# Kernel tuning notes

Hardware: AMD Instinct MI355X
Metric: run time of the kernel (lower is better)

Reference implementation:

```python
import jax, jax.numpy as jnp
import numpy as np

F = 32          # fmap_size = (256 // 16) * 2
WIN = F // 8 - 1  # window = 3
HID = 160
HID4 = 640
N = 4096
Q = 16


def setup_inputs() -> dict:
    key = jax.random.key(0)
    ks = jax.random.split(key, 24)

    def lin(k, i, o):
        return jax.random.normal(k, (i, o), jnp.float32) * (1.0 / np.sqrt(i))

    return {
        "feature_pos": jax.random.normal(ks[0], (N, Q, HID), jnp.float32),
        "query_embedding": jax.random.normal(ks[1], (N, Q, HID), jnp.float32),
        "attn_matrix": jax.random.normal(ks[2], (N, Q, F * F), jnp.float32),
        "ws1": lin(ks[3], HID, HID4), "bs1": jnp.zeros((HID4,), jnp.float32),
        "ws2": lin(ks[4], HID4, HID4), "bs2": jnp.zeros((HID4,), jnp.float32),
        "ws3": lin(ks[5], HID4, HID4), "bs3": jnp.zeros((HID4,), jnp.float32),
        "ws4": lin(ks[6], HID4, 1), "bs4": jnp.zeros((1,), jnp.float32),
        "wp1": lin(ks[7], HID, HID4), "bp1": jnp.zeros((HID4,), jnp.float32),
        "wp2": lin(ks[8], HID4, HID4), "bp2": jnp.zeros((HID4,), jnp.float32),
        "wp3": lin(ks[9], HID4, HID4), "bp3": jnp.zeros((HID4,), jnp.float32),
        "wp4": lin(ks[10], HID4, 4), "bp4": jnp.zeros((4,), jnp.float32),
    }


def _mlp(x, w1, b1, w2, b2, w3, b3, w4, b4):
    h = jax.nn.relu(x @ w1 + b1)
    h = jax.nn.relu(h @ w2 + b2)
    h = jax.nn.relu(h @ w3 + b3)
    return h @ w4 + b4


def _gauss_blur3(x):
    # torchvision GaussianBlur(3, sigma=1.0): separable 3-tap, reflect padding
    e = np.exp(-0.5)
    k = jnp.asarray([e, 1.0, e], jnp.float32) / np.float32(1.0 + 2.0 * e)
    xp = jnp.pad(x, ((0, 0), (1, 1), (0, 0)), mode="reflect")
    x = k[0] * xp[:, :-2] + k[1] * xp[:, 1:-1] + k[2] * xp[:, 2:]
    xp = jnp.pad(x, ((0, 0), (0, 0), (1, 1)), mode="reflect")
    return k[0] * xp[:, :, :-2] + k[1] * xp[:, :, 1:-1] + k[2] * xp[:, :, 2:]


def _process_attnmap(am):
    # am: [N, F, F]
    n = am.shape[0]
    ab = _gauss_blur3(am)
    ab = (ab - ab.mean(axis=(1, 2), keepdims=True)) / jnp.std(ab, axis=(1, 2), keepdims=True, ddof=1)
    idx = jnp.argmax(ab.reshape(n, -1), axis=1)
    px = (idx % F).astype(jnp.int32)
    py = (idx // F).astype(jnp.int32)
    # vectorized windowed mean of clamped sigmoid (masked instead of per-sample slicing)
    s = jnp.clip(jax.nn.sigmoid(am), 1e-4, 1.0 - 1e-4)
    pos = jnp.arange(F)
    colmask = ((pos[None, :] >= jnp.maximum(0, px - WIN)[:, None]) &
               (pos[None, :] < jnp.minimum(F, px + WIN)[:, None])).astype(s.dtype)  # [N,F]
    rowmask = ((pos[None, :] >= jnp.maximum(0, py - WIN)[:, None]) &
               (pos[None, :] < jnp.minimum(F, py + WIN)[:, None])).astype(s.dtype)
    colsum = s.sum(axis=1)  # [N,F] sum over rows -> per-column totals
    rowsum = s.sum(axis=2)  # [N,F] sum over cols -> per-row totals
    tempx = (colsum * colmask).sum(axis=1) / (F * colmask.sum(axis=1))
    tempy = (rowsum * rowmask).sum(axis=1) / (F * rowmask.sum(axis=1))
    prepos = jnp.stack([px, py], axis=1).astype(jnp.float32)          # [N,2]
    presize = jnp.stack([tempx, tempy], axis=1) * np.float32(F)        # [N,2]
    return prepos, presize


def reference(feature_pos, query_embedding, attn_matrix,
              ws1, bs1, ws2, bs2, ws3, bs3, ws4, bs4,
              wp1, bp1, wp2, bp2, wp3, bp3, wp4, bp4):
    n = query_embedding.shape[0]
    qe = query_embedding.mean(axis=1)   # [N, HID]
    fp = feature_pos.mean(axis=1)       # [N, HID]
    am = attn_matrix.mean(axis=1).reshape(n, F, F)
    score = _mlp(qe, ws1, bs1, ws2, bs2, ws3, bs3, ws4, bs4).reshape(n)
    bbox_info = _mlp(fp, wp1, bp1, wp2, bp2, wp3, bp3, wp4, bp4)  # [N,4]
    sizeoffset = jnp.clip(bbox_info[:, :2], -2.0, 2.0)
    posoffset = jnp.clip(bbox_info[:, 2:], -2.0, 2.0)
    prepos, presize = _process_attnmap(am)
    xy = (prepos + posoffset) / np.float32(F)
    wh = (presize + sizeoffset) / np.float32(F)
    xy = xy - 0.5 * wh  # predict_center
    bbox = jnp.concatenate([xy, wh], axis=1)
    return bbox, score
```

## Files before the change

kernel.cpp:

```cpp
#include <hip/hip_runtime.h>
#include <hip/hip_bf16.h>
#include <stdint.h>

#define HID 160
#define HID4 640
#define FDIM 32
#define NPIX 1024

#define GK0 0.27406862f
#define GK1 0.45186276f

typedef __attribute__((ext_vector_type(8))) short short8;
typedef __attribute__((ext_vector_type(4))) float f32x4;

__device__ __forceinline__ ushort f2b(float f) {
  union { float f; uint32_t u; } v; v.f = f;
  uint32_t u = v.u;
  u += 0x7fffu + ((u >> 16) & 1u);
  return (ushort)(u >> 16);
}
__device__ __forceinline__ float b2f(ushort s) {
  union { uint32_t u; float f; } v; v.u = ((uint32_t)s) << 16;
  return v.f;
}

__device__ __forceinline__ void gload16(const ushort* g, ushort* l) {
  __builtin_amdgcn_global_load_lds(
      (const __attribute__((address_space(1))) void*)g,
      (__attribute__((address_space(3))) void*)l, 16, 0, 0);
}

union SMem {
  struct {
    ushort la[128 * 32];
    ushort lb[128 * 32];
  } g;
  struct {
    float am[FDIM][FDIM + 1];
    float tmp[FDIM][FDIM + 1];
    float bl[FDIM][FDIM + 1];
    float rowsum[FDIM], colsum[FDIM];
    float redv[4];
    int redi[4];
  } a;
};

__device__ void attn_block(SMem& sm, const float* __restrict__ attn,
                           float* __restrict__ pp, int n) {
  const int tid = threadIdx.x;
  const float* base = attn + (size_t)n * (16 * NPIX);
  float4 a = make_float4(0.f, 0.f, 0.f, 0.f);
#pragma unroll
  for (int q = 0; q < 16; ++q) {
    float4 v = *(const float4*)(base + q * NPIX + tid * 4);
    a.x += v.x; a.y += v.y; a.z += v.z; a.w += v.w;
  }
  {
    const int f0 = tid * 4;
    const int r = f0 >> 5, c = f0 & 31;
    sm.a.am[r][c + 0] = a.x * 0.0625f;
    sm.a.am[r][c + 1] = a.y * 0.0625f;
    sm.a.am[r][c + 2] = a.z * 0.0625f;
    sm.a.am[r][c + 3] = a.w * 0.0625f;
  }
  __syncthreads();
  for (int f = tid; f < NPIX; f += 256) {
    int r = f >> 5, c = f & 31;
    int rm = (r == 0) ? 1 : r - 1;
    int rp = (r == 31) ? 30 : r + 1;
    sm.a.tmp[r][c] = GK0 * sm.a.am[rm][c] + GK1 * sm.a.am[r][c] + GK0 * sm.a.am[rp][c];
  }
  __syncthreads();
  for (int f = tid; f < NPIX; f += 256) {
    int r = f >> 5, c = f & 31;
    int cm = (c == 0) ? 1 : c - 1;
    int cp = (c == 31) ? 30 : c + 1;
    sm.a.bl[r][c] = GK0 * sm.a.tmp[r][cm] + GK1 * sm.a.tmp[r][c] + GK0 * sm.a.tmp[r][cp];
  }
  __syncthreads();
  float bv = -1e30f; int bi = 0;
  for (int f = tid; f < NPIX; f += 256) {
    float v = sm.a.bl[f >> 5][f & 31];
    if (v > bv || (v == bv && f < bi)) { bv = v; bi = f; }
  }
  for (int off = 32; off > 0; off >>= 1) {
    float ov = __shfl_down(bv, off);
    int oi = __shfl_down(bi, off);
    if (ov > bv || (ov == bv && oi < bi)) { bv = ov; bi = oi; }
  }
  if ((tid & 63) == 0) { sm.a.redv[tid >> 6] = bv; sm.a.redi[tid >> 6] = bi; }
  for (int f = tid; f < NPIX; f += 256) {
    int r = f >> 5, c = f & 31;
    float s = 1.f / (1.f + expf(-sm.a.am[r][c]));
    sm.a.tmp[r][c] = fminf(fmaxf(s, 1e-4f), 0.9999f);
  }
  __syncthreads();
  if (tid < 32) {
    float s = 0.f;
    for (int c = 0; c < 32; ++c) s += sm.a.tmp[tid][c];
    sm.a.rowsum[tid] = s;
  } else if (tid < 64) {
    int c = tid - 32;
    float s = 0.f;
    for (int r = 0; r < 32; ++r) s += sm.a.tmp[r][c];
    sm.a.colsum[c] = s;
  }
  __syncthreads();
  if (tid == 0) {
    float bestv = sm.a.redv[0]; int besti = sm.a.redi[0];
    for (int w = 1; w < 4; ++w)
      if (sm.a.redv[w] > bestv || (sm.a.redv[w] == bestv && sm.a.redi[w] < besti)) {
        bestv = sm.a.redv[w]; besti = sm.a.redi[w];
      }
    int px = besti & 31, py = besti >> 5;
    int c0 = max(0, px - 3), c1 = min(32, px + 3);
    float sx = 0.f;
    for (int c = c0; c < c1; ++c) sx += sm.a.colsum[c];
    float psx = (sx / (32.f * (float)(c1 - c0))) * 32.f;
    int r0 = max(0, py - 3), r1 = min(32, py + 3);
    float sy = 0.f;
    for (int r = r0; r < r1; ++r) sy += sm.a.rowsum[r];
    float psy = (sy / (32.f * (float)(r1 - r0))) * 32.f;
    pp[n * 4 + 0] = (float)px;
    pp[n * 4 + 1] = (float)py;
    pp[n * 4 + 2] = psx;
    pp[n * 4 + 3] = psy;
  }
}

template <int K>
__global__ __launch_bounds__(256) void gemm_attn(
    const ushort* __restrict__ A0, const ushort* __restrict__ A1,
    const ushort* __restrict__ W0, const ushort* __restrict__ W1,
    const float* __restrict__ B0, const float* __restrict__ B1,
    ushort* __restrict__ O0, ushort* __restrict__ O1,
    const float* __restrict__ attn, float* __restrict__ pp,
    int attn_base, int n_gemm) {
  __shared__ SMem sm;
  const int tid = threadIdx.x;

  if ((int)blockIdx.x >= n_gemm) {
    attn_block(sm, attn, pp, attn_base + (int)blockIdx.x - n_gemm);
    return;
  }

  const int bid = blockIdx.x;
  const int half = n_gemm >> 1;
  const int chain = bid >= half;
  const int r = chain ? bid - half : bid;
  const int bn = (r % 5) * 128;
  const int bm = (r / 5) * 128;
  const ushort* A = chain ? A1 : A0;
  const ushort* W = chain ? W1 : W0;
  const float* bias = chain ? B1 : B0;
  ushort* O = chain ? O1 : O0;

  const int lane = tid & 63;
  const int wid = tid >> 6;
  const int wr = (wid >> 1) * 64;
  const int wc = (wid & 1) * 64;
  const int l15 = lane & 15;
  const int kq = (lane >> 4) * 8;

  const int rstage = tid >> 2;
  const int cstage = (tid & 3) * 8;
  ushort* la = sm.g.la;
  ushort* lb = sm.g.lb;
  const int ldsbase = wid * 512;

  f32x4 acc[4][4] = {};
  for (int k0 = 0; k0 < K; k0 += 32) {
#pragma unroll
    for (int j = 0; j < 2; ++j) {
      gload16(A + (size_t)(bm + j * 64 + rstage) * K + k0 + cstage,
              la + j * 2048 + ldsbase);
      gload16(W + (size_t)(bn + j * 64 + rstage) * K + k0 + cstage,
              lb + j * 2048 + ldsbase);
    }
    __syncthreads();
    short8 af[4], bf[4];
#pragma unroll
    for (int i = 0; i < 4; ++i) {
      af[i] = *(const short8*)(la + (wr + i * 16 + l15) * 32 + kq);
      bf[i] = *(const short8*)(lb + (wc + i * 16 + l15) * 32 + kq);
    }
#pragma unroll
    for (int mi = 0; mi < 4; ++mi)
#pragma unroll
      for (int nj = 0; nj < 4; ++nj)
        acc[mi][nj] = __builtin_amdgcn_mfma_f32_16x16x32_bf16(af[mi], bf[nj], acc[mi][nj], 0, 0, 0);
    __syncthreads();
  }

#pragma unroll
  for (int nj = 0; nj < 4; ++nj) {
    const int col = bn + wc + nj * 16 + l15;
    const float bcol = bias[col];
#pragma unroll
    for (int mi = 0; mi < 4; ++mi) {
      const int rbase = bm + wr + mi * 16 + (lane >> 4) * 4;
#pragma unroll
      for (int b = 0; b < 4; ++b) {
        float v = acc[mi][nj][b] + bcol;
        O[(size_t)(rbase + b) * HID4 + col] = f2b(fmaxf(v, 0.f));
      }
    }
  }
}

__global__ __launch_bounds__(256) void prep_kernel(
    const float* __restrict__ qemb, const float* __restrict__ fpos,
    ushort* __restrict__ qe_b, ushort* __restrict__ fp_b,
    const float* __restrict__ ws1, ushort* __restrict__ wts1,
    const float* __restrict__ wp1, ushort* __restrict__ wtp1,
    const float* __restrict__ ws2, ushort* __restrict__ wts2,
    const float* __restrict__ wp2, ushort* __restrict__ wtp2,
    const float* __restrict__ ws3, ushort* __restrict__ wts3,
    const float* __restrict__ wp3, ushort* __restrict__ wtp3,
    int n_mean_blocks, int total) {
  const int tid = threadIdx.x;
  const int bid = blockIdx.x;

  if (bid < n_mean_blocks) {
    int idx = bid * 256 + tid;
    const int pairs = total >> 1;
    const float* src; ushort* dst; int i;
    if (idx < pairs) { src = qemb; dst = qe_b; i = idx; }
    else             { src = fpos; dst = fp_b; i = idx - pairs; }
    int nn = i / (HID / 2);
    int h = (i - nn * (HID / 2)) * 2;
    const float* p = src + (size_t)nn * (16 * HID) + h;
    float sx = 0.f, sy = 0.f;
#pragma unroll
    for (int q = 0; q < 16; ++q) {
      float2 v = *(const float2*)(p + q * HID);
      sx += v.x; sy += v.y;
    }
    ushort2 o;
    o.x = f2b(sx * 0.0625f);
    o.y = f2b(sy * 0.0625f);
    *(ushort2*)(dst + (size_t)nn * HID + h) = o;
    return;
  }

  int r = bid - n_mean_blocks;
  const float* in; ushort* out; int K;
  if (r < 100)       { in = ws1; out = wts1; K = HID; }
  else if (r < 200)  { in = wp1; out = wtp1; K = HID; r -= 100; }
  else if (r < 600)  { in = ws2; out = wts2; K = HID4; r -= 200; }
  else if (r < 1000) { in = wp2; out = wtp2; K = HID4; r -= 600; }
  else if (r < 1400) { in = ws3; out = wts3; K = HID4; r -= 1000; }
  else               { in = wp3; out = wtp3; K = HID4; r -= 1400; }
  const int bx = (r % 20) * 32;
  const int by = (r / 20) * 32;
  const int lx = tid & 31;
  const int ly = tid >> 5;
  __shared__ float t[32][33];
#pragma unroll
  for (int i = 0; i < 4; ++i)
    t[ly + i * 8][lx] = in[(size_t)(by + ly + i * 8) * HID4 + bx + lx];
  __syncthreads();
#pragma unroll
  for (int i = 0; i < 4; ++i)
    out[(size_t)(bx + ly + i * 8) * K + by + lx] = f2b(t[lx][ly + i * 8]);
}

__global__ __launch_bounds__(256) void final_kernel(
    const ushort* __restrict__ hs, const ushort* __restrict__ hp,
    const float* __restrict__ ws4, const float* __restrict__ bs4,
    const float* __restrict__ wp4, const float* __restrict__ bp4,
    const float* __restrict__ pp, float* __restrict__ out, int N) {
  const int wid = threadIdx.x >> 6;
  const int lane = threadIdx.x & 63;
  const int n = blockIdx.x * 4 + wid;
  if (n >= N) return;
  const ushort* hsr = hs + (size_t)n * HID4;
  const ushort* hpr = hp + (size_t)n * HID4;
  float sc = 0.f, b0 = 0.f, b1 = 0.f, b2 = 0.f, b3 = 0.f;
  for (int j = lane; j < HID4; j += 64) {
    float h1 = b2f(hsr[j]);
    sc += h1 * ws4[j];
    float h2 = b2f(hpr[j]);
    b0 += h2 * wp4[j * 4 + 0];
    b1 += h2 * wp4[j * 4 + 1];
    b2 += h2 * wp4[j * 4 + 2];
    b3 += h2 * wp4[j * 4 + 3];
  }
  for (int off = 32; off > 0; off >>= 1) {
    sc += __shfl_down(sc, off);
    b0 += __shfl_down(b0, off);
    b1 += __shfl_down(b1, off);
    b2 += __shfl_down(b2, off);
    b3 += __shfl_down(b3, off);
  }
  if (lane == 0) {
    sc += bs4[0];
    b0 += bp4[0]; b1 += bp4[1]; b2 += bp4[2]; b3 += bp4[3];
    float so0 = fminf(fmaxf(b0, -2.f), 2.f);
    float so1 = fminf(fmaxf(b1, -2.f), 2.f);
    float po0 = fminf(fmaxf(b2, -2.f), 2.f);
    float po1 = fminf(fmaxf(b3, -2.f), 2.f);
    float px = pp[n * 4 + 0], py = pp[n * 4 + 1];
    float psx = pp[n * 4 + 2], psy = pp[n * 4 + 3];
    float wh0 = (psx + so0) * (1.f / 32.f);
    float wh1 = (psy + so1) * (1.f / 32.f);
    float xy0 = (px + po0) * (1.f / 32.f) - 0.5f * wh0;
    float xy1 = (py + po1) * (1.f / 32.f) - 0.5f * wh1;
    out[n * 4 + 0] = xy0;
    out[n * 4 + 1] = xy1;
    out[n * 4 + 2] = wh0;
    out[n * 4 + 3] = wh1;
    out[(size_t)4 * N + n] = sc;
  }
}

extern "C" void kernel_launch(void* const* d_in, const int* in_sizes, int n_in,
                              void* d_out, int out_size, void* d_ws, size_t ws_size,
                              hipStream_t stream) {
  const float* fpos = (const float*)d_in[0];
  const float* qemb = (const float*)d_in[1];
  const float* attn = (const float*)d_in[2];
  const float* ws1 = (const float*)d_in[3];
  const float* bs1 = (const float*)d_in[4];
  const float* ws2 = (const float*)d_in[5];
  const float* bs2 = (const float*)d_in[6];
  const float* ws3 = (const float*)d_in[7];
  const float* bs3 = (const float*)d_in[8];
  const float* ws4 = (const float*)d_in[9];
  const float* bs4 = (const float*)d_in[10];
  const float* wp1 = (const float*)d_in[11];
  const float* bp1 = (const float*)d_in[12];
  const float* wp2 = (const float*)d_in[13];
  const float* bp2 = (const float*)d_in[14];
  const float* wp3 = (const float*)d_in[15];
  const float* bp3 = (const float*)d_in[16];
  const float* wp4 = (const float*)d_in[17];
  const float* bp4 = (const float*)d_in[18];
  float* out = (float*)d_out;

  const int N = in_sizes[0] / (16 * HID);

  char* ws = (char*)d_ws;
  const size_t SZ_QE = (size_t)N * HID * 2;
  const size_t SZ_W1 = (size_t)HID4 * HID * 2;
  const size_t SZ_W2 = (size_t)HID4 * HID4 * 2;
  const size_t SZ_H  = (size_t)N * HID4 * 2;
  size_t off = 0;
  ushort* qe_b = (ushort*)(ws + off); off += SZ_QE;
  ushort* fp_b = (ushort*)(ws + off); off += SZ_QE;
  ushort* wts1 = (ushort*)(ws + off); off += SZ_W1;
  ushort* wtp1 = (ushort*)(ws + off); off += SZ_W1;
  ushort* wts2 = (ushort*)(ws + off); off += SZ_W2;
  ushort* wtp2 = (ushort*)(ws + off); off += SZ_W2;
  ushort* wts3 = (ushort*)(ws + off); off += SZ_W2;
  ushort* wtp3 = (ushort*)(ws + off); off += SZ_W2;
  ushort* hsA  = (ushort*)(ws + off); off += SZ_H;
  ushort* hsB  = (ushort*)(ws + off); off += SZ_H;
  ushort* hpA  = (ushort*)(ws + off); off += SZ_H;
  ushort* hpB  = (ushort*)(ws + off); off += SZ_H;
  float*  pp   = (float*)(ws + off);  off += (size_t)N * 4 * 4;

  const int total = N * HID;
  const int n_mean_blocks = (2 * (total >> 1) + 255) / 256;
  prep_kernel<<<n_mean_blocks + 1800, 256, 0, stream>>>(
      qemb, fpos, qe_b, fp_b, ws1, wts1, wp1, wtp1, ws2, wts2, wp2, wtp2,
      ws3, wts3, wp3, wtp3, n_mean_blocks, total);

  const int n_gemm = 2 * 5 * (N / 128);
  const int a2 = (N * 29) / 100;
  const int a3 = a2;
  const int a1 = N - a2 - a3;

  gemm_attn<HID><<<n_gemm + a1, 256, 0, stream>>>(
      qe_b, fp_b, wts1, wtp1, bs1, bp1, hsA, hpA, attn, pp, 0, n_gemm);
  gemm_attn<HID4><<<n_gemm + a2, 256, 0, stream>>>(
      hsA, hpA, wts2, wtp2, bs2, bp2, hsB, hpB, attn, pp, a1, n_gemm);
  gemm_attn<HID4><<<n_gemm + a3, 256, 0, stream>>>(
      hsB, hpB, wts3, wtp3, bs3, bp3, hsA, hpA, attn, pp, a1 + a2, n_gemm);

  final_kernel<<<(N + 3) / 4, 256, 0, stream>>>(hsA, hpA, ws4, bs4, wp4, bp4, pp, out, N);
}
```

Measured before the change: 119.4 us.

## Double-buffer GEMM LDS loads, swizzle layout, halve N tile, rebalance attn blocks

The GEMM main loop now double-buffers its LDS tiles, issuing the next K-slice's global-to-LDS loads before computing on the current one and using explicit waitcnt plus barriers. It also XOR-swizzles the LDS layout to cut bank conflicts and shrinks the N tile from 128 to 64, which doubles the GEMM block count. The attention-map blocks are redistributed across four launches, with a share moved into the prep kernel. The cost is more LDS per block and more A-tile reloads, in exchange for better latency hiding and load balance.

```diff
diff --git a/kernel.cpp b/kernel.cpp
--- a/kernel.cpp
+++ b/kernel.cpp
@@ -30,22 +30,29 @@
       (__attribute__((address_space(3))) void*)l, 16, 0, 0);
 }
 
-union SMem {
+struct AttnSM {
+  float am[FDIM][FDIM + 1];
+  float tmp[FDIM][FDIM + 1];
+  float bl[FDIM][FDIM + 1];
+  float rowsum[FDIM], colsum[FDIM];
+  float redv[4];
+  int redi[4];
+};
+
+union GemmSM {
   struct {
-    ushort la[128 * 32];
-    ushort lb[128 * 32];
+    ushort la[2][4096];
+    ushort lb[2][2048];
   } g;
-  struct {
-    float am[FDIM][FDIM + 1];
-    float tmp[FDIM][FDIM + 1];
-    float bl[FDIM][FDIM + 1];
-    float rowsum[FDIM], colsum[FDIM];
-    float redv[4];
-    int redi[4];
-  } a;
+  AttnSM a;
 };
 
-__device__ void attn_block(SMem& sm, const float* __restrict__ attn,
+union PrepSM {
+  float t[32][33];
+  AttnSM a;
+};
+
+__device__ void attn_block(AttnSM& sm, const float* __restrict__ attn,
                            float* __restrict__ pp, int n) {
   const int tid = threadIdx.x;
   const float* base = attn + (size_t)n * (16 * NPIX);
@@ -58,29 +65,29 @@
   {
     const int f0 = tid * 4;
     const int r = f0 >> 5, c = f0 & 31;
-    sm.a.am[r][c + 0] = a.x * 0.0625f;
-    sm.a.am[r][c + 1] = a.y * 0.0625f;
-    sm.a.am[r][c + 2] = a.z * 0.0625f;
-    sm.a.am[r][c + 3] = a.w * 0.0625f;
+    sm.am[r][c + 0] = a.x * 0.0625f;
+    sm.am[r][c + 1] = a.y * 0.0625f;
+    sm.am[r][c + 2] = a.z * 0.0625f;
+    sm.am[r][c + 3] = a.w * 0.0625f;
   }
   __syncthreads();
   for (int f = tid; f < NPIX; f += 256) {
     int r = f >> 5, c = f & 31;
     int rm = (r == 0) ? 1 : r - 1;
     int rp = (r == 31) ? 30 : r + 1;
-    sm.a.tmp[r][c] = GK0 * sm.a.am[rm][c] + GK1 * sm.a.am[r][c] + GK0 * sm.a.am[rp][c];
+    sm.tmp[r][c] = GK0 * sm.am[rm][c] + GK1 * sm.am[r][c] + GK0 * sm.am[rp][c];
   }
   __syncthreads();
   for (int f = tid; f < NPIX; f += 256) {
     int r = f >> 5, c = f & 31;
     int cm = (c == 0) ? 1 : c - 1;
     int cp = (c == 31) ? 30 : c + 1;
-    sm.a.bl[r][c] = GK0 * sm.a.tmp[r][cm] + GK1 * sm.a.tmp[r][c] + GK0 * sm.a.tmp[r][cp];
+    sm.bl[r][c] = GK0 * sm.tmp[r][cm] + GK1 * sm.tmp[r][c] + GK0 * sm.tmp[r][cp];
   }
   __syncthreads();
   float bv = -1e30f; int bi = 0;
   for (int f = tid; f < NPIX; f += 256) {
-    float v = sm.a.bl[f >> 5][f & 31];
+    float v = sm.bl[f >> 5][f & 31];
     if (v > bv || (v == bv && f < bi)) { bv = v; bi = f; }
   }
   for (int off = 32; off > 0; off >>= 1) {
@@ -88,38 +95,38 @@
     int oi = __shfl_down(bi, off);
     if (ov > bv || (ov == bv && oi < bi)) { bv = ov; bi = oi; }
   }
-  if ((tid & 63) == 0) { sm.a.redv[tid >> 6] = bv; sm.a.redi[tid >> 6] = bi; }
+  if ((tid & 63) == 0) { sm.redv[tid >> 6] = bv; sm.redi[tid >> 6] = bi; }
   for (int f = tid; f < NPIX; f += 256) {
     int r = f >> 5, c = f & 31;
-    float s = 1.f / (1.f + expf(-sm.a.am[r][c]));
-    sm.a.tmp[r][c] = fminf(fmaxf(s, 1e-4f), 0.9999f);
+    float s = 1.f / (1.f + expf(-sm.am[r][c]));
+    sm.tmp[r][c] = fminf(fmaxf(s, 1e-4f), 0.9999f);
   }
   __syncthreads();
   if (tid < 32) {
     float s = 0.f;
-    for (int c = 0; c < 32; ++c) s += sm.a.tmp[tid][c];
-    sm.a.rowsum[tid] = s;
+    for (int c = 0; c < 32; ++c) s += sm.tmp[tid][c];
+    sm.rowsum[tid] = s;
   } else if (tid < 64) {
     int c = tid - 32;
     float s = 0.f;
-    for (int r = 0; r < 32; ++r) s += sm.a.tmp[r][c];
-    sm.a.colsum[c] = s;
+    for (int r = 0; r < 32; ++r) s += sm.tmp[r][c];
+    sm.colsum[c] = s;
   }
   __syncthreads();
   if (tid == 0) {
-    float bestv = sm.a.redv[0]; int besti = sm.a.redi[0];
+    float bestv = sm.redv[0]; int besti = sm.redi[0];
     for (int w = 1; w < 4; ++w)
-      if (sm.a.redv[w] > bestv || (sm.a.redv[w] == bestv && sm.a.redi[w] < besti)) {
-        bestv = sm.a.redv[w]; besti = sm.a.redi[w];
+      if (sm.redv[w] > bestv || (sm.redv[w] == bestv && sm.redi[w] < besti)) {
+        bestv = sm.redv[w]; besti = sm.redi[w];
       }
     int px = besti & 31, py = besti >> 5;
     int c0 = max(0, px - 3), c1 = min(32, px + 3);
     float sx = 0.f;
-    for (int c = c0; c < c1; ++c) sx += sm.a.colsum[c];
+    for (int c = c0; c < c1; ++c) sx += sm.colsum[c];
     float psx = (sx / (32.f * (float)(c1 - c0))) * 32.f;
     int r0 = max(0, py - 3), r1 = min(32, py + 3);
     float sy = 0.f;
-    for (int r = r0; r < r1; ++r) sy += sm.a.rowsum[r];
+    for (int r = r0; r < r1; ++r) sy += sm.rowsum[r];
     float psy = (sy / (32.f * (float)(r1 - r0))) * 32.f;
     pp[n * 4 + 0] = (float)px;
     pp[n * 4 + 1] = (float)py;
@@ -136,11 +143,11 @@
     ushort* __restrict__ O0, ushort* __restrict__ O1,
     const float* __restrict__ attn, float* __restrict__ pp,
     int attn_base, int n_gemm) {
-  __shared__ SMem sm;
+  __shared__ GemmSM sm;
   const int tid = threadIdx.x;
 
   if ((int)blockIdx.x >= n_gemm) {
-    attn_block(sm, attn, pp, attn_base + (int)blockIdx.x - n_gemm);
+    attn_block(sm.a, attn, pp, attn_base + (int)blockIdx.x - n_gemm);
     return;
   }
 
@@ -148,8 +155,8 @@
   const int half = n_gemm >> 1;
   const int chain = bid >= half;
   const int r = chain ? bid - half : bid;
-  const int bn = (r % 5) * 128;
-  const int bm = (r / 5) * 128;
+  const int bn = (r % 10) * 64;
+  const int bm = (r / 10) * 128;
   const ushort* A = chain ? A1 : A0;
   const ushort* W = chain ? W1 : W0;
   const float* bias = chain ? B1 : B0;
@@ -158,42 +165,67 @@
   const int lane = tid & 63;
   const int wid = tid >> 6;
   const int wr = (wid >> 1) * 64;
-  const int wc = (wid & 1) * 64;
+  const int wc = (wid & 1) * 32;
   const int l15 = lane & 15;
   const int kq = (lane >> 4) * 8;
 
   const int rstage = tid >> 2;
   const int cstage = (tid & 3) * 8;
-  ushort* la = sm.g.la;
-  ushort* lb = sm.g.lb;
-  const int ldsbase = wid * 512;
-
-  f32x4 acc[4][4] = {};
-  for (int k0 = 0; k0 < K; k0 += 32) {
-#pragma unroll
-    for (int j = 0; j < 2; ++j) {
-      gload16(A + (size_t)(bm + j * 64 + rstage) * K + k0 + cstage,
-              la + j * 2048 + ldsbase);
-      gload16(W + (size_t)(bn + j * 64 + rstage) * K + k0 + cstage,
-              lb + j * 2048 + ldsbase);
+  const int cs_sw = cstage ^ ((rstage & 6) << 2);
+
+  ushort* la = &sm.g.la[0][0];
+  ushort* lb = &sm.g.lb[0][0];
+  const int ldsw = wid * 512;
+
+  const size_t arow0 = (size_t)(bm + rstage) * K + cs_sw;
+  const size_t arow1 = (size_t)(bm + 64 + rstage) * K + cs_sw;
+  const size_t brow  = (size_t)(bn + rstage) * K + cs_sw;
+
+  gload16(A + arow0, la + ldsw);
+  gload16(A + arow1, la + 2048 + ldsw);
+  gload16(W + brow,  lb + ldsw);
+
+  constexpr int NT = K / 32;
+  f32x4 acc[4][2] = {};
+  for (int t = 0; t < NT; ++t) {
+    const int cur = t & 1;
+    if (t + 1 < NT) {
+      const int k1 = (t + 1) * 32;
+      const int nxt = cur ^ 1;
+      gload16(A + arow0 + k1, la + nxt * 4096 + ldsw);
+      gload16(A + arow1 + k1, la + nxt * 4096 + 2048 + ldsw);
+      gload16(W + brow + k1,  lb + nxt * 2048 + ldsw);
+      asm volatile("s_waitcnt vmcnt(3)" ::: "memory");
+    } else {
+      asm volatile("s_waitcnt vmcnt(0)" ::: "memory");
     }
-    __syncthreads();
-    short8 af[4], bf[4];
-#pragma unroll
-    for (int i = 0; i < 4; ++i) {
-      af[i] = *(const short8*)(la + (wr + i * 16 + l15) * 32 + kq);
-      bf[i] = *(const short8*)(lb + (wc + i * 16 + l15) * 32 + kq);
+    __builtin_amdgcn_s_barrier();
+
+    const ushort* lac = la + cur * 4096;
+    const ushort* lbc = lb + cur * 2048;
+    short8 af[4], bf[2];
+#pragma unroll
+    for (int mi = 0; mi < 4; ++mi) {
+      const int rr = wr + mi * 16 + l15;
+      af[mi] = *(const short8*)(lac + rr * 32 + (kq ^ ((rr & 6) << 2)));
     }
 #pragma unroll
+    for (int nj = 0; nj < 2; ++nj) {
+      const int rr = wc + nj * 16 + l15;
+      bf[nj] = *(const short8*)(lbc + rr * 32 + (kq ^ ((rr & 6) << 2)));
+    }
+#pragma unroll
     for (int mi = 0; mi < 4; ++mi)
 #pragma unroll
-      for (int nj = 0; nj < 4; ++nj)
+      for (int nj = 0; nj < 2; ++nj)
         acc[mi][nj] = __builtin_amdgcn_mfma_f32_16x16x32_bf16(af[mi], bf[nj], acc[mi][nj], 0, 0, 0);
-    __syncthreads();
-  }
-
-#pragma unroll
-  for (int nj = 0; nj < 4; ++nj) {
+
+    asm volatile("s_waitcnt lgkmcnt(0)" ::: "memory");
+    __builtin_amdgcn_s_barrier();
+  }
+
+#pragma unroll
+  for (int nj = 0; nj < 2; ++nj) {
     const int col = bn + wc + nj * 16 + l15;
     const float bcol = bias[col];
 #pragma unroll
@@ -217,7 +249,9 @@
     const float* __restrict__ wp2, ushort* __restrict__ wtp2,
     const float* __restrict__ ws3, ushort* __restrict__ wts3,
     const float* __restrict__ wp3, ushort* __restrict__ wtp3,
-    int n_mean_blocks, int total) {
+    const float* __restrict__ attn, float* __restrict__ pp,
+    int n_mean_blocks, int n_trans_blocks, int total) {
+  __shared__ PrepSM sm;
   const int tid = threadIdx.x;
   const int bid = blockIdx.x;
 
@@ -243,26 +277,30 @@
     return;
   }
 
-  int r = bid - n_mean_blocks;
-  const float* in; ushort* out; int K;
-  if (r < 100)       { in = ws1; out = wts1; K = HID; }
-  else if (r < 200)  { in = wp1; out = wtp1; K = HID; r -= 100; }
-  else if (r < 600)  { in = ws2; out = wts2; K = HID4; r -= 200; }
-  else if (r < 1000) { in = wp2; out = wtp2; K = HID4; r -= 600; }
-  else if (r < 1400) { in = ws3; out = wts3; K = HID4; r -= 1000; }
-  else               { in = wp3; out = wtp3; K = HID4; r -= 1400; }
-  const int bx = (r % 20) * 32;
-  const int by = (r / 20) * 32;
-  const int lx = tid & 31;
-  const int ly = tid >> 5;
-  __shared__ float t[32][33];
-#pragma unroll
-  for (int i = 0; i < 4; ++i)
-    t[ly + i * 8][lx] = in[(size_t)(by + ly + i * 8) * HID4 + bx + lx];
-  __syncthreads();
-#pragma unroll
-  for (int i = 0; i < 4; ++i)
-    out[(size_t)(bx + ly + i * 8) * K + by + lx] = f2b(t[lx][ly + i * 8]);
+  if (bid < n_mean_blocks + n_trans_blocks) {
+    int r = bid - n_mean_blocks;
+    const float* in; ushort* out; int K;
+    if (r < 100)       { in = ws1; out = wts1; K = HID; }
+    else if (r < 200)  { in = wp1; out = wtp1; K = HID; r -= 100; }
+    else if (r < 600)  { in = ws2; out = wts2; K = HID4; r -= 200; }
+    else if (r < 1000) { in = wp2; out = wtp2; K = HID4; r -= 600; }
+    else if (r < 1400) { in = ws3; out = wts3; K = HID4; r -= 1000; }
+    else               { in = wp3; out = wtp3; K = HID4; r -= 1400; }
+    const int bx = (r % 20) * 32;
+    const int by = (r / 20) * 32;
+    const int lx = tid & 31;
+    const int ly = tid >> 5;
+#pragma unroll
+    for (int i = 0; i < 4; ++i)
+      sm.t[ly + i * 8][lx] = in[(size_t)(by + ly + i * 8) * HID4 + bx + lx];
+    __syncthreads();
+#pragma unroll
+    for (int i = 0; i < 4; ++i)
+      out[(size_t)(bx + ly + i * 8) * K + by + lx] = f2b(sm.t[lx][ly + i * 8]);
+    return;
+  }
+
+  attn_block(sm.a, attn, pp, bid - n_mean_blocks - n_trans_blocks);
 }
 
 __global__ __launch_bounds__(256) void final_kernel(
@@ -360,23 +398,26 @@
   ushort* hpB  = (ushort*)(ws + off); off += SZ_H;
   float*  pp   = (float*)(ws + off);  off += (size_t)N * 4 * 4;
 
+  const int a0 = (N * 25) / 64;
+  const int a1 = (N * 11) / 64;
+  const int a2 = (N * 14) / 64;
+  const int a3 = N - a0 - a1 - a2;
+
   const int total = N * HID;
-  const int n_mean_blocks = (2 * (total >> 1) + 255) / 256;
-  prep_kernel<<<n_mean_blocks + 1800, 256, 0, stream>>>(
+  const int n_mean = (total + 255) / 256;
+  const int n_trans = 1800;
+  prep_kernel<<<n_mean + n_trans + a0, 256, 0, stream>>>(
       qemb, fpos, qe_b, fp_b, ws1, wts1, wp1, wtp1, ws2, wts2, wp2, wtp2,
-      ws3, wts3, wp3, wtp3, n_mean_blocks, total);
-
-  const int n_gemm = 2 * 5 * (N / 128);
-  const int a2 = (N * 29) / 100;
-  const int a3 = a2;
-  const int a1 = N - a2 - a3;
+      ws3, wts3, wp3, wtp3, attn, pp, n_mean, n_trans, total);
+
+  const int n_gemm = 2 * (N / 128) * (HID4 / 64);
 
   gemm_attn<HID><<<n_gemm + a1, 256, 0, stream>>>(
-      qe_b, fp_b, wts1, wtp1, bs1, bp1, hsA, hpA, attn, pp, 0, n_gemm);
+      qe_b, fp_b, wts1, wtp1, bs1, bp1, hsA, hpA, attn, pp, a0, n_gemm);
   gemm_attn<HID4><<<n_gemm + a2, 256, 0, stream>>>(
-      hsA, hpA, wts2, wtp2, bs2, bp2, hsB, hpB, attn, pp, a1, n_gemm);
+      hsA, hpA, wts2, wtp2, bs2, bp2, hsB, hpB, attn, pp, a0 + a1, n_gemm);
   gemm_attn<HID4><<<n_gemm + a3, 256, 0, stream>>>(
-      hsB, hpB, wts3, wtp3, bs3, bp3, hsA, hpA, attn, pp, a1 + a2, n_gemm);
+      hsB, hpB, wts3, wtp3, bs3, bp3, hsA, hpA, attn, pp, a0 + a1 + a2, n_gemm);
 
   final_kernel<<<(N + 3) / 4, 256, 0, stream>>>(hsA, hpA, ws4, bs4, wp4, bp4, pp, out, N);
 }
```

After: 131.8 us. 10.4% more time.

## Process four attention maps per block with register prefetch of the next map

Applied to the files above, without the earlier changes.

Each attention block now handles four consecutive samples instead of one. While the current map is being processed in shared memory, the block loads the next sample's 16 query rows into registers, so global loads overlap with the blur, argmax and sigmoid work. This cuts the number of attention blocks by four and amortises per-block launch overhead, but it raises register pressure (16 float4 buffers) and lengthens each block's serial work, which could hurt overlap with the co-scheduled GEMM blocks. The remaining edits are cosmetic reorganisation of shared memory and launch arithmetic.

```diff
diff --git a/kernel.cpp b/kernel.cpp
--- a/kernel.cpp
+++ b/kernel.cpp
@@ -30,101 +30,130 @@
       (__attribute__((address_space(3))) void*)l, 16, 0, 0);
 }
 
-union SMem {
+struct AttnSM {
+  float am[FDIM][FDIM + 1];
+  float tmp[FDIM][FDIM + 1];
+  float bl[FDIM][FDIM + 1];
+  float rowsum[FDIM], colsum[FDIM];
+  float redv[4];
+  int redi[4];
+};
+
+union GemmSM {
   struct {
     ushort la[128 * 32];
     ushort lb[128 * 32];
   } g;
-  struct {
-    float am[FDIM][FDIM + 1];
-    float tmp[FDIM][FDIM + 1];
-    float bl[FDIM][FDIM + 1];
-    float rowsum[FDIM], colsum[FDIM];
-    float redv[4];
-    int redi[4];
-  } a;
+  AttnSM a;
 };
 
-__device__ void attn_block(SMem& sm, const float* __restrict__ attn,
-                           float* __restrict__ pp, int n) {
+__device__ void attn_multi(AttnSM& sm, const float* __restrict__ attn,
+                           float* __restrict__ pp, int n0, int cnt) {
   const int tid = threadIdx.x;
-  const float* base = attn + (size_t)n * (16 * NPIX);
-  float4 a = make_float4(0.f, 0.f, 0.f, 0.f);
-#pragma unroll
-  for (int q = 0; q < 16; ++q) {
-    float4 v = *(const float4*)(base + q * NPIX + tid * 4);
-    a.x += v.x; a.y += v.y; a.z += v.z; a.w += v.w;
-  }
+  float4 buf[16];
   {
-    const int f0 = tid * 4;
-    const int r = f0 >> 5, c = f0 & 31;
-    sm.a.am[r][c + 0] = a.x * 0.0625f;
-    sm.a.am[r][c + 1] = a.y * 0.0625f;
-    sm.a.am[r][c + 2] = a.z * 0.0625f;
-    sm.a.am[r][c + 3] = a.w * 0.0625f;
-  }
-  __syncthreads();
-  for (int f = tid; f < NPIX; f += 256) {
-    int r = f >> 5, c = f & 31;
-    int rm = (r == 0) ? 1 : r - 1;
-    int rp = (r == 31) ? 30 : r + 1;
-    sm.a.tmp[r][c] = GK0 * sm.a.am[rm][c] + GK1 * sm.a.am[r][c] + GK0 * sm.a.am[rp][c];
-  }
-  __syncthreads();
-  for (int f = tid; f < NPIX; f += 256) {
-    int r = f >> 5, c = f & 31;
-    int cm = (c == 0) ? 1 : c - 1;
-    int cp = (c == 31) ? 30 : c + 1;
-    sm.a.bl[r][c] = GK0 * sm.a.tmp[r][cm] + GK1 * sm.a.tmp[r][c] + GK0 * sm.a.tmp[r][cp];
-  }
-  __syncthreads();
-  float bv = -1e30f; int bi = 0;
-  for (int f = tid; f < NPIX; f += 256) {
-    float v = sm.a.bl[f >> 5][f & 31];
-    if (v > bv || (v == bv && f < bi)) { bv = v; bi = f; }
-  }
-  for (int off = 32; off > 0; off >>= 1) {
-    float ov = __shfl_down(bv, off);
-    int oi = __shfl_down(bi, off);
-    if (ov > bv || (ov == bv && oi < bi)) { bv = ov; bi = oi; }
-  }
-  if ((tid & 63) == 0) { sm.a.redv[tid >> 6] = bv; sm.a.redi[tid >> 6] = bi; }
-  for (int f = tid; f < NPIX; f += 256) {
-    int r = f >> 5, c = f & 31;
-    float s = 1.f / (1.f + expf(-sm.a.am[r][c]));
-    sm.a.tmp[r][c] = fminf(fmaxf(s, 1e-4f), 0.9999f);
-  }
-  __syncthreads();
-  if (tid < 32) {
-    float s = 0.f;
-    for (int c = 0; c < 32; ++c) s += sm.a.tmp[tid][c];
-    sm.a.rowsum[tid] = s;
-  } else if (tid < 64) {
-    int c = tid - 32;
-    float s = 0.f;
-    for (int r = 0; r < 32; ++r) s += sm.a.tmp[r][c];
-    sm.a.colsum[c] = s;
-  }
-  __syncthreads();
-  if (tid == 0) {
-    float bestv = sm.a.redv[0]; int besti = sm.a.redi[0];
-    for (int w = 1; w < 4; ++w)
-      if (sm.a.redv[w] > bestv || (sm.a.redv[w] == bestv && sm.a.redi[w] < besti)) {
-        bestv = sm.a.redv[w]; besti = sm.a.redi[w];
-      }
-    int px = besti & 31, py = besti >> 5;
-    int c0 = max(0, px - 3), c1 = min(32, px + 3);
-    float sx = 0.f;
-    for (int c = c0; c < c1; ++c) sx += sm.a.colsum[c];
-    float psx = (sx / (32.f * (float)(c1 - c0))) * 32.f;
-    int r0 = max(0, py - 3), r1 = min(32, py + 3);
-    float sy = 0.f;
-    for (int r = r0; r < r1; ++r) sy += sm.a.rowsum[r];
-    float psy = (sy / (32.f * (float)(r1 - r0))) * 32.f;
-    pp[n * 4 + 0] = (float)px;
-    pp[n * 4 + 1] = (float)py;
-    pp[n * 4 + 2] = psx;
-    pp[n * 4 + 3] = psy;
+    const float* b0 = attn + (size_t)n0 * (16 * NPIX) + tid * 4;
+#pragma unroll
+    for (int q = 0; q < 16; ++q) buf[q] = *(const float4*)(b0 + q * NPIX);
+  }
+
+  for (int s = 0; s < cnt; ++s) {
+    float4 a;
+#pragma unroll
+    for (int q = 8; q < 16; ++q) {
+      buf[q - 8].x += buf[q].x; buf[q - 8].y += buf[q].y;
+      buf[q - 8].z += buf[q].z; buf[q - 8].w += buf[q].w;
+    }
+#pragma unroll
+    for (int q = 4; q < 8; ++q) {
+      buf[q - 4].x += buf[q].x; buf[q - 4].y += buf[q].y;
+      buf[q - 4].z += buf[q].z; buf[q - 4].w += buf[q].w;
+    }
+    a.x = (buf[0].x + buf[2].x) + (buf[1].x + buf[3].x);
+    a.y = (buf[0].y + buf[2].y) + (buf[1].y + buf[3].y);
+    a.z = (buf[0].z + buf[2].z) + (buf[1].z + buf[3].z);
+    a.w = (buf[0].w + buf[2].w) + (buf[1].w + buf[3].w);
+
+    {
+      const int f0 = tid * 4;
+      const int r = f0 >> 5, c = f0 & 31;
+      sm.am[r][c + 0] = a.x * 0.0625f;
+      sm.am[r][c + 1] = a.y * 0.0625f;
+      sm.am[r][c + 2] = a.z * 0.0625f;
+      sm.am[r][c + 3] = a.w * 0.0625f;
+    }
+    __syncthreads();
+
+    if (s + 1 < cnt) {
+      const float* nb = attn + (size_t)(n0 + s + 1) * (16 * NPIX) + tid * 4;
+#pragma unroll
+      for (int q = 0; q < 16; ++q) buf[q] = *(const float4*)(nb + q * NPIX);
+    }
+
+    const int n = n0 + s;
+    for (int f = tid; f < NPIX; f += 256) {
+      int r = f >> 5, c = f & 31;
+      int rm = (r == 0) ? 1 : r - 1;
+      int rp = (r == 31) ? 30 : r + 1;
+      sm.tmp[r][c] = GK0 * sm.am[rm][c] + GK1 * sm.am[r][c] + GK0 * sm.am[rp][c];
+    }
+    __syncthreads();
+    for (int f = tid; f < NPIX; f += 256) {
+      int r = f >> 5, c = f & 31;
+      int cm = (c == 0) ? 1 : c - 1;
+      int cp = (c == 31) ? 30 : c + 1;
+      sm.bl[r][c] = GK0 * sm.tmp[r][cm] + GK1 * sm.tmp[r][c] + GK0 * sm.tmp[r][cp];
+    }
+    __syncthreads();
+    float bv = -1e30f; int bi = 0;
+    for (int f = tid; f < NPIX; f += 256) {
+      float v = sm.bl[f >> 5][f & 31];
+      if (v > bv || (v == bv && f < bi)) { bv = v; bi = f; }
+    }
+    for (int off = 32; off > 0; off >>= 1) {
+      float ov = __shfl_down(bv, off);
+      int oi = __shfl_down(bi, off);
+      if (ov > bv || (ov == bv && oi < bi)) { bv = ov; bi = oi; }
+    }
+    if ((tid & 63) == 0) { sm.redv[tid >> 6] = bv; sm.redi[tid >> 6] = bi; }
+    for (int f = tid; f < NPIX; f += 256) {
+      int r = f >> 5, c = f & 31;
+      float sg = 1.f / (1.f + expf(-sm.am[r][c]));
+      sm.tmp[r][c] = fminf(fmaxf(sg, 1e-4f), 0.9999f);
+    }
+    __syncthreads();
+    if (tid < 32) {
+      float ss = 0.f;
+      for (int c = 0; c < 32; ++c) ss += sm.tmp[tid][c];
+      sm.rowsum[tid] = ss;
+    } else if (tid < 64) {
+      int c = tid - 32;
+      float ss = 0.f;
+      for (int r = 0; r < 32; ++r) ss += sm.tmp[r][c];
+      sm.colsum[c] = ss;
+    }
+    __syncthreads();
+    if (tid == 0) {
+      float bestv = sm.redv[0]; int besti = sm.redi[0];
+      for (int w = 1; w < 4; ++w)
+        if (sm.redv[w] > bestv || (sm.redv[w] == bestv && sm.redi[w] < besti)) {
+          bestv = sm.redv[w]; besti = sm.redi[w];
+        }
+      int px = besti & 31, py = besti >> 5;
+      int c0 = max(0, px - 3), c1 = min(32, px + 3);
+      float sx = 0.f;
+      for (int c = c0; c < c1; ++c) sx += sm.colsum[c];
+      float psx = (sx / (32.f * (float)(c1 - c0))) * 32.f;
+      int r0 = max(0, py - 3), r1 = min(32, py + 3);
+      float sy = 0.f;
+      for (int r = r0; r < r1; ++r) sy += sm.rowsum[r];
+      float psy = (sy / (32.f * (float)(r1 - r0))) * 32.f;
+      pp[n * 4 + 0] = (float)px;
+      pp[n * 4 + 1] = (float)py;
+      pp[n * 4 + 2] = psx;
+      pp[n * 4 + 3] = psy;
+    }
+    __syncthreads();
   }
 }
 
@@ -135,12 +164,14 @@
     const float* __restrict__ B0, const float* __restrict__ B1,
     ushort* __restrict__ O0, ushort* __restrict__ O1,
     const float* __restrict__ attn, float* __restrict__ pp,
-    int attn_base, int n_gemm) {
-  __shared__ SMem sm;
+    int attn_base, int attn_cnt, int n_gemm) {
+  __shared__ GemmSM sm;
   const int tid = threadIdx.x;
 
   if ((int)blockIdx.x >= n_gemm) {
-    attn_block(sm, attn, pp, attn_base + (int)blockIdx.x - n_gemm);
+    const int n0 = attn_base + ((int)blockIdx.x - n_gemm) * 4;
+    const int cnt = min(4, attn_base + attn_cnt - n0);
+    attn_multi(sm.a, attn, pp, n0, cnt);
     return;
   }
 
@@ -218,6 +249,7 @@
     const float* __restrict__ ws3, ushort* __restrict__ wts3,
     const float* __restrict__ wp3, ushort* __restrict__ wtp3,
     int n_mean_blocks, int total) {
+  __shared__ float t[32][33];
   const int tid = threadIdx.x;
   const int bid = blockIdx.x;
 
@@ -255,7 +287,6 @@
   const int by = (r / 20) * 32;
   const int lx = tid & 31;
   const int ly = tid >> 5;
-  __shared__ float t[32][33];
 #pragma unroll
   for (int i = 0; i < 4; ++i)
     t[ly + i * 8][lx] = in[(size_t)(by + ly + i * 8) * HID4 + bx + lx];
@@ -361,22 +392,27 @@
   float*  pp   = (float*)(ws + off);  off += (size_t)N * 4 * 4;
 
   const int total = N * HID;
-  const int n_mean_blocks = (2 * (total >> 1) + 255) / 256;
-  prep_kernel<<<n_mean_blocks + 1800, 256, 0, stream>>>(
+  const int n_mean = (total + 255) / 256;
+  const int n_trans = 1800;
+  prep_kernel<<<n_mean + n_trans, 256, 0, stream>>>(
       qemb, fpos, qe_b, fp_b, ws1, wts1, wp1, wtp1, ws2, wts2, wp2, wtp2,
-      ws3, wts3, wp3, wtp3, n_mean_blocks, total);
-
-  const int n_gemm = 2 * 5 * (N / 128);
+      ws3, wts3, wp3, wtp3, n_mean, total);
+
+  const int n_gemm = 2 * (N / 128) * (HID4 / 128);
+
   const int a2 = (N * 29) / 100;
   const int a3 = a2;
   const int a1 = N - a2 - a3;
-
-  gemm_attn<HID><<<n_gemm + a1, 256, 0, stream>>>(
-      qe_b, fp_b, wts1, wtp1, bs1, bp1, hsA, hpA, attn, pp, 0, n_gemm);
-  gemm_attn<HID4><<<n_gemm + a2, 256, 0, stream>>>(
-      hsA, hpA, wts2, wtp2, bs2, bp2, hsB, hpB, attn, pp, a1, n_gemm);
-  gemm_attn<HID4><<<n_gemm + a3, 256, 0, stream>>>(
-      hsB, hpB, wts3, wtp3, bs3, bp3, hsA, hpA, attn, pp, a1 + a2, n_gemm);
+  const int nb1 = (a1 + 3) / 4;
+  const int nb2 = (a2 + 3) / 4;
+  const int nb3 = (a3 + 3) / 4;
+
+  gemm_attn<HID><<<n_gemm + nb1, 256, 0, stream>>>(
+      qe_b, fp_b, wts1, wtp1, bs1, bp1, hsA, hpA, attn, pp, 0, a1, n_gemm);
+  gemm_attn<HID4><<<n_gemm + nb2, 256, 0, stream>>>(
+      hsA, hpA, wts2, wtp2, bs2, bp2, hsB, hpB, attn, pp, a1, a2, n_gemm);
+  gemm_attn<HID4><<<n_gemm + nb3, 256, 0, stream>>>(
+      hsB, hpB, wts3, wtp3, bs3, bp3, hsA, hpA, attn, pp, a1 + a2, a3, n_gemm);
 
   final_kernel<<<(N + 3) / 4, 256, 0, stream>>>(hsA, hpA, ws4, bs4, wp4, bp4, pp, out, N);
 }
```

Result: slower. 193.3 us (+62.0%).
